# Kernel tuning notes

Measured on AMD Instinct MI355X. Metric: run time of the kernel, lower is better.

Reference implementation:

```python
import jax, jax.numpy as jnp
import numpy as np

B, S, HID = 8, 1024, 1024
NH, HD = 16, 64  # num heads, head dim; NH*HD == HID


def setup_inputs() -> dict:
    key = jax.random.key(0)
    ks = jax.random.split(key, 8)
    sc = 0.02
    return {
        "hidden_states": jax.random.normal(ks[0], (B, S, HID), jnp.float32),
        "attention_mask": jnp.zeros((B, 1, 1, S), jnp.float32),
        "Wq": jax.random.normal(ks[1], (HID, HID), jnp.float32) * sc,
        "bq": jnp.zeros((HID,), jnp.float32),
        "Wk": jax.random.normal(ks[2], (HID, HID), jnp.float32) * sc,
        "bk": jnp.zeros((HID,), jnp.float32),
        "Wv": jax.random.normal(ks[3], (HID, HID), jnp.float32) * sc,
        "bv": jnp.zeros((HID,), jnp.float32),
    }


def reference(hidden_states, attention_mask, Wq, bq, Wk, bk, Wv, bv):
    def split_heads(x):  # [B,S,HID] -> [B,NH,S,HD]
        return x.reshape(B, S, NH, HD).transpose(0, 2, 1, 3)

    q = split_heads(hidden_states @ Wq + bq)
    k = split_heads(hidden_states @ Wk + bk)
    v = split_heads(hidden_states @ Wv + bv)

    # [B,NH,S,S] score matrix, scale, additive mask, softmax
    scores = jnp.einsum("bhqd,bhkd->bhqk", q, k) / jnp.sqrt(jnp.float32(HD))
    scores = scores + attention_mask
    probs = jax.nn.softmax(scores, axis=-1)  # dropout prob = 0.0 -> identity

    ctx = jnp.einsum("bhqk,bhkd->bhqd", probs, v)
    return ctx.transpose(0, 2, 1, 3).reshape(B, S, HID)
```

## Files before the change

### kernel.cpp

```cpp
#include <hip/hip_runtime.h>


typedef __bf16 bf16x8 __attribute__((ext_vector_type(8)));
typedef float f32x16 __attribute__((ext_vector_type(16)));

__device__ __forceinline__ unsigned rne16(float x) {
  unsigned u = __builtin_bit_cast(unsigned, x);
  return (u + 0x7fffu + ((u >> 16) & 1u)) >> 16;
}
__device__ __forceinline__ unsigned packbf(float lo, float hi) {
  return rne16(lo) | (rne16(hi) << 16);
}
__device__ __forceinline__ unsigned packbf_fast(float lo, float hi) {
  unsigned ul = __builtin_bit_cast(unsigned, lo) + 0x8000u;
  unsigned uh = __builtin_bit_cast(unsigned, hi) + 0x8000u;
  return __builtin_amdgcn_perm(uh, ul, 0x07060302u);
}
__device__ __forceinline__ void async16(void* l, const void* g) {
  __builtin_amdgcn_global_load_lds((const __attribute__((address_space(1))) void*)g,
                                   (__attribute__((address_space(3))) void*)l, 16, 0, 0);
}

__global__ __launch_bounds__(256) void k_prep(const float* __restrict__ h,
                                              unsigned short* __restrict__ hbf,
                                              const float* __restrict__ Wq,
                                              const float* __restrict__ Wk,
                                              const float* __restrict__ Wv,
                                              unsigned short* __restrict__ wt) {
  __shared__ float t[32][33];
  int bid = blockIdx.x, tid = threadIdx.x;
  if (bid < 8192) {
    size_t i = (size_t)bid * 256 + tid;
    float4 v = ((const float4*)h)[i];
    uint2 r;
    r.x = packbf(v.x, v.y);
    r.y = packbf(v.z, v.w);
    ((uint2*)hbf)[i] = r;
  } else {
    int id = bid - 8192;
    int which = id >> 10;
    int sub = id & 1023;
    int c0 = (sub & 31) * 32, k0 = (sub >> 5) * 32;
    const float* W = which == 0 ? Wq : (which == 1 ? Wk : Wv);
    int tx = tid & 31, ty = tid >> 5;
#pragma unroll
    for (int i = 0; i < 4; ++i) {
      int r = ty + i * 8;
      t[r][tx] = W[(size_t)(k0 + r) * 1024 + c0 + tx];
    }
    __syncthreads();
#pragma unroll
    for (int i = 0; i < 4; ++i) {
      int r = ty + i * 8;
      wt[((size_t)which * 1024 + c0 + r) * 1024 + k0 + tx] = (unsigned short)rne16(t[tx][r]);
    }
  }
}

__global__ __launch_bounds__(256, 2) void k_gemm(const unsigned short* __restrict__ A,
                                                 const unsigned short* __restrict__ Bm,
                                                 const float* __restrict__ bq,
                                                 const float* __restrict__ bk,
                                                 const float* __restrict__ bv,
                                                 unsigned short* __restrict__ qkv,
                                                 unsigned short* __restrict__ vt) {
  __shared__ __align__(16) char lds[49152];
  int tid = threadIdx.x, w = tid >> 6, lane = tid & 63, l5 = lane & 31, q5 = lane >> 5;
  int wr = w >> 1, wc = w & 1;
  int m0 = blockIdx.x * 256, n0 = blockIdx.y * 128;

  f32x16 acc[4][2];
#pragma unroll
  for (int i = 0; i < 4; ++i)
#pragma unroll
    for (int j = 0; j < 2; ++j)
#pragma unroll
      for (int e = 0; e < 16; ++e) acc[i][j][e] = 0.f;

  auto stage = [&](int kt, char* buf) {
    int k0 = kt * 32;
#pragma unroll
    for (int t = 0; t < 6; ++t) {
      int idx = w * 6 + t;
      if (idx < 16) {
        int mt = idx >> 1, ks = idx & 1;
        async16(buf + idx * 1024,
                A + (size_t)(m0 + mt * 32 + l5) * 1024 + k0 + ks * 16 + q5 * 8);
      } else {
        int i2 = idx - 16, nt = i2 >> 1, ks = i2 & 1;
        async16(buf + 16384 + i2 * 1024,
                Bm + (size_t)(n0 + nt * 32 + l5) * 1024 + k0 + ks * 16 + q5 * 8);
      }
    }
  };

  auto compute = [&](const char* buf) {
#pragma unroll
    for (int ks = 0; ks < 2; ++ks) {
      bf16x8 b0 = *(const bf16x8*)(buf + 16384 + ((wc * 2 + 0) * 2 + ks) * 1024 + lane * 16);
      bf16x8 b1 = *(const bf16x8*)(buf + 16384 + ((wc * 2 + 1) * 2 + ks) * 1024 + lane * 16);
#pragma unroll
      for (int mt = 0; mt < 4; ++mt) {
        bf16x8 a = *(const bf16x8*)(buf + ((wr * 4 + mt) * 2 + ks) * 1024 + lane * 16);
        acc[mt][0] = __builtin_amdgcn_mfma_f32_32x32x16_bf16(a, b0, acc[mt][0], 0, 0, 0);
        acc[mt][1] = __builtin_amdgcn_mfma_f32_32x32x16_bf16(a, b1, acc[mt][1], 0, 0, 0);
      }
    }
  };

  char* buf0 = lds;
  char* buf1 = lds + 24576;
  stage(0, buf0);
#pragma unroll 1
  for (int kt = 0; kt < 32; kt += 2) {
    __syncthreads();
    if (kt + 1 < 32) stage(kt + 1, buf1);
    compute(buf0);
    __syncthreads();
    if (kt + 2 < 32) stage(kt + 2, buf0);
    compute(buf1);
  }

  int which = n0 >> 10;
  if (which != 2) {
    const float* bp = which == 0 ? bq : bk;
    unsigned short* dst = qkv + (size_t)which * 8388608;
#pragma unroll
    for (int nt = 0; nt < 2; ++nt) {
      int n_in = (n0 & 1023) + wc * 64 + nt * 32 + l5;
      float bias = bp[n_in];
      int hh = n_in >> 6, d = n_in & 63;
#pragma unroll
      for (int mt = 0; mt < 4; ++mt) {
#pragma unroll
        for (int e = 0; e < 16; ++e) {
          int m = m0 + wr * 128 + mt * 32 + (e & 3) + 8 * (e >> 2) + 4 * q5;
          int b = m >> 10, s = m & 1023;
          dst[((size_t)(b * 16 + hh) << 16) + (s << 6) + d] =
              (unsigned short)rne16(acc[mt][nt][e] + bias);
        }
      }
    }
  } else {
    int b = m0 >> 10;
    unsigned short* scr = (unsigned short*)(lds) + w * 2176;
#pragma unroll
    for (int mt = 0; mt < 4; ++mt) {
#pragma unroll
      for (int nt = 0; nt < 2; ++nt) {
        int n_in = (n0 & 1023) + wc * 64 + nt * 32 + l5;
        float bias = bv[n_in];
        unsigned short* tile = scr + nt * 1088;
#pragma unroll
        for (int jj = 0; jj < 8; ++jj) {
          int e = 2 * jj;
          int s_loc = (e & 3) + 8 * (e >> 2) + 4 * q5;
          *(unsigned*)(tile + l5 * 34 + s_loc) =
              packbf(acc[mt][nt][e] + bias, acc[mt][nt][e + 1] + bias);
        }
      }
#pragma unroll
      for (int nt = 0; nt < 2; ++nt) {
        const unsigned short* tile = scr + nt * 1088;
        unsigned di[8];
#pragma unroll
        for (int i = 0; i < 8; ++i)
          di[i] = *(const unsigned*)(tile + l5 * 34 + q5 * 16 + i * 2);
        int n_in = (n0 & 1023) + wc * 64 + nt * 32 + l5;
        int hh = n_in >> 6, dd = n_in & 63;
        int s_base = (m0 & 1023) + wr * 128 + mt * 32 + q5 * 16;
        unsigned short* dst = vt + ((size_t)(b * 16 + hh) * 64 + dd) * 1024 + s_base;
        uint4 v0 = {di[0], di[1], di[2], di[3]};
        uint4 v1 = {di[4], di[5], di[6], di[7]};
        *(uint4*)(dst) = v0;
        *(uint4*)(dst + 8) = v1;
      }
    }
  }
}

__global__ __launch_bounds__(256, 4) void k_attn(const unsigned short* __restrict__ qg,
                                                 const unsigned short* __restrict__ kg,
                                                 const unsigned short* __restrict__ vtg,
                                                 const float* __restrict__ maskg,
                                                 float* __restrict__ out) {
  __shared__ __align__(16) char lds[36864];
  char* KF = lds;
  char* VF = lds + 16384;
  float* MK = (float*)(lds + 32768);
  int tid = threadIdx.x, w = tid >> 6, lane = tid & 63, l5 = lane & 31, q5 = lane >> 5;
  int idx = blockIdx.x;
  int bi = idx & 7;
  int j = idx >> 3;
  int h = j >> 3, qc = j & 7;
  int bh = bi * 16 + h, s0 = qc * 128;
  const unsigned short* qb = qg + ((size_t)bh << 16);
  const unsigned short* kb = kg + ((size_t)bh << 16);
  const unsigned short* vb = vtg + ((size_t)bh << 16);
  const float LG = 1.4426950408889634f;
  const float C1 = 0.125f * LG;

  {
    float4 mv = *(const float4*)(maskg + (size_t)bi * 1024 + tid * 4);
    mv.x *= LG; mv.y *= LG; mv.z *= LG; mv.w *= LG;
    *(float4*)(MK + tid * 4) = mv;
  }

  bf16x8 qfr[4];
#pragma unroll
  for (int ds = 0; ds < 4; ++ds)
    qfr[ds] = *(const bf16x8*)(qb + (size_t)(s0 + w * 32 + l5) * 64 + ds * 16 + q5 * 8);

  f32x16 O[2];
#pragma unroll
  for (int i = 0; i < 2; ++i)
#pragma unroll
    for (int e = 0; e < 16; ++e) O[i][e] = 0.f;
  float lsum = 0.f;

#pragma unroll 1
  for (int kt = 0; kt < 8; ++kt) {
    int k0 = kt * 128;
    __syncthreads();
#pragma unroll
    for (int t = 0; t < 4; ++t) {
      int f = w * 4 + t, mt = f >> 2, ds = f & 3;
      async16(KF + f * 1024, kb + (size_t)(k0 + mt * 32 + l5) * 64 + ds * 16 + q5 * 8);
    }
#pragma unroll
    for (int t = 0; t < 4; ++t) {
      int f = w * 4 + t, dt = f >> 3, ks = f & 7;
      async16(VF + f * 1024, vb + (size_t)(dt * 32 + l5) * 1024 + k0 + ks * 16 + q5 * 8);
    }
    __syncthreads();

#pragma unroll
    for (int mt = 0; mt < 4; ++mt) {
      f32x16 S;
#pragma unroll
      for (int e = 0; e < 16; ++e) S[e] = 0.f;
#pragma unroll
      for (int ds = 0; ds < 4; ++ds) {
        bf16x8 a = *(const bf16x8*)(KF + (mt * 4 + ds) * 1024 + lane * 16);
        S = __builtin_amdgcn_mfma_f32_32x32x16_bf16(a, qfr[ds], S, 0, 0, 0);
      }
      float p[16];
#pragma unroll
      for (int g4 = 0; g4 < 4; ++g4) {
        float4 mv = *(const float4*)(MK + k0 + mt * 32 + g4 * 8 + q5 * 4);
        p[g4 * 4 + 0] = __builtin_amdgcn_exp2f(S[g4 * 4 + 0] * C1 + mv.x);
        p[g4 * 4 + 1] = __builtin_amdgcn_exp2f(S[g4 * 4 + 1] * C1 + mv.y);
        p[g4 * 4 + 2] = __builtin_amdgcn_exp2f(S[g4 * 4 + 2] * C1 + mv.z);
        p[g4 * 4 + 3] = __builtin_amdgcn_exp2f(S[g4 * 4 + 3] * C1 + mv.w);
      }
      unsigned p2[8];
#pragma unroll
      for (int e = 0; e < 16; ++e) lsum += p[e];
#pragma unroll
      for (int jj = 0; jj < 8; ++jj) p2[jj] = packbf_fast(p[2 * jj], p[2 * jj + 1]);
#pragma unroll
      for (int kh = 0; kh < 2; ++kh) {
        int ks = mt * 2 + kh, gp = kh * 4;
        bf16x8 av0 = *(const bf16x8*)(VF + (0 * 8 + ks) * 1024 + lane * 16);
        bf16x8 av1 = *(const bf16x8*)(VF + (1 * 8 + ks) * 1024 + lane * 16);
        unsigned o0 = p2[gp + 0], o1 = p2[gp + 1];
        unsigned o2 = p2[gp + 2], o3 = p2[gp + 3];
        unsigned t0 = __shfl_xor((int)o0, 32);
        unsigned t1 = __shfl_xor((int)o1, 32);
        unsigned t2 = __shfl_xor((int)o2, 32);
        unsigned t3 = __shfl_xor((int)o3, 32);
        uint4 fu;
        fu.x = q5 ? t2 : o0;
        fu.y = q5 ? t3 : o1;
        fu.z = q5 ? o2 : t0;
        fu.w = q5 ? o3 : t1;
        bf16x8 bfrag = __builtin_bit_cast(bf16x8, fu);
        O[0] = __builtin_amdgcn_mfma_f32_32x32x16_bf16(av0, bfrag, O[0], 0, 0, 0);
        O[1] = __builtin_amdgcn_mfma_f32_32x32x16_bf16(av1, bfrag, O[1], 0, 0, 0);
      }
    }
  }

  __syncthreads();
  float* Ob = (float*)(lds + w * 8192);
  float lt = lsum + __shfl_xor(lsum, 32);
  float rinv = 1.0f / lt;
#pragma unroll
  for (int dt = 0; dt < 2; ++dt)
#pragma unroll
    for (int g4 = 0; g4 < 4; ++g4) {
      float4 val;
      val.x = O[dt][g4 * 4 + 0] * rinv;
      val.y = O[dt][g4 * 4 + 1] * rinv;
      val.z = O[dt][g4 * 4 + 2] * rinv;
      val.w = O[dt][g4 * 4 + 3] * rinv;
      int c = dt * 8 + g4 * 2 + q5;
      *(float4*)(Ob + l5 * 64 + (c ^ (l5 & 15)) * 4) = val;
    }
#pragma unroll
  for (int t = 0; t < 8; ++t) {
    int qr = t * 4 + (lane >> 4), cr = lane & 15;
    float4 vv = *(const float4*)(Ob + qr * 64 + (cr ^ (qr & 15)) * 4);
    int s = s0 + w * 32 + qr;
    *(float4*)(out + (((size_t)(bi * 1024 + s)) << 10) + (h << 6) + (cr << 2)) = vv;
  }
}

extern "C" void kernel_launch(void* const* d_in, const int* in_sizes, int n_in,
                              void* d_out, int out_size, void* d_ws, size_t ws_size,
                              hipStream_t stream) {
  (void)in_sizes; (void)n_in; (void)out_size; (void)ws_size;
  const float* hidden = (const float*)d_in[0];
  const float* mask = (const float*)d_in[1];
  const float* Wq = (const float*)d_in[2];
  const float* bq = (const float*)d_in[3];
  const float* Wk = (const float*)d_in[4];
  const float* bk = (const float*)d_in[5];
  const float* Wv = (const float*)d_in[6];
  const float* bv = (const float*)d_in[7];
  float* out = (float*)d_out;
  char* ws = (char*)d_ws;
  unsigned short* hbf = (unsigned short*)ws;
  unsigned short* wt  = (unsigned short*)(ws + 16777216);
  unsigned short* qkv = (unsigned short*)(ws + 23068672);
  unsigned short* vt  = (unsigned short*)(ws + 56623104);

  k_prep<<<11264, 256, 0, stream>>>(hidden, hbf, Wq, Wk, Wv, wt);
  k_gemm<<<dim3(32, 24), 256, 0, stream>>>(hbf, wt, bq, bk, bv, qkv, vt);
  k_attn<<<1024, 256, 0, stream>>>(qkv, qkv + 8388608, vt, mask, out);
}
```

Baseline: 254.1 us.

## Rewrite QKV GEMM with 256x256 tiles, 512 threads and swizzled LDS pipelining

The QKV projection GEMM now uses 256x256 output tiles per 512-thread block with 16x16x32 MFMAs. Operands are staged through a 128KB double-buffered, XOR-swizzled LDS layout with interleaved async prefetches, explicit waitcnt/barrier scheduling and setprio around the MFMA bursts. It also remaps block IDs for XCD locality and simplifies the V-transpose epilogue to direct packed stores. This raises data reuse per LDS byte and overlaps loads with compute, at the cost of heavy LDS use that limits occupancy and hand-tuned synchronization that is fragile.

Result: faster. 220.9 us (-13.0%).

```diff
diff --git a/kernel.cpp b/kernel.cpp
--- a/kernel.cpp
+++ b/kernel.cpp
@@ -2,7 +2,9 @@
 
 
 typedef __bf16 bf16x8 __attribute__((ext_vector_type(8)));
+typedef float f32x4 __attribute__((ext_vector_type(4)));
 typedef float f32x16 __attribute__((ext_vector_type(16)));
+typedef int i32x4 __attribute__((ext_vector_type(4)));
 
 __device__ __forceinline__ unsigned rne16(float x) {
   unsigned u = __builtin_bit_cast(unsigned, x);
@@ -19,6 +21,12 @@
 __device__ __forceinline__ void async16(void* l, const void* g) {
   __builtin_amdgcn_global_load_lds((const __attribute__((address_space(1))) void*)g,
                                    (__attribute__((address_space(3))) void*)l, 16, 0, 0);
+}
+__device__ __forceinline__ bf16x8 dsr128(const char* p) {
+  i32x4 r;
+  unsigned a = (unsigned)(size_t)(const __attribute__((address_space(3))) char*)p;
+  asm volatile("ds_read_b128 %0, %1" : "=v"(r) : "v"(a));
+  return __builtin_bit_cast(bf16x8, r);
 }
 
 __global__ __launch_bounds__(256) void k_prep(const float* __restrict__ h,
@@ -57,123 +65,154 @@
   }
 }
 
-__global__ __launch_bounds__(256, 2) void k_gemm(const unsigned short* __restrict__ A,
+__global__ __launch_bounds__(512, 2) void k_gemm(const unsigned short* __restrict__ A,
                                                  const unsigned short* __restrict__ Bm,
                                                  const float* __restrict__ bq,
                                                  const float* __restrict__ bk,
                                                  const float* __restrict__ bv,
                                                  unsigned short* __restrict__ qkv,
                                                  unsigned short* __restrict__ vt) {
-  __shared__ __align__(16) char lds[49152];
-  int tid = threadIdx.x, w = tid >> 6, lane = tid & 63, l5 = lane & 31, q5 = lane >> 5;
-  int wr = w >> 1, wc = w & 1;
-  int m0 = blockIdx.x * 256, n0 = blockIdx.y * 128;
-
-  f32x16 acc[4][2];
-#pragma unroll
-  for (int i = 0; i < 4; ++i)
+  __shared__ __align__(16) char lds[131072];
+  const int tid = threadIdx.x;
+  const int w = tid >> 6, lane = tid & 63;
+  const int wm = w >> 2, wn = w & 3;
+
+  int orig = blockIdx.x;
+  int wgid = (orig & 7) * 48 + (orig >> 3);
+  int tm = wgid / 12, tn = wgid - tm * 12;
+  int m0 = tm * 256, n0 = tn * 256;
+
+  int ro[2], ke[2];
+#pragma unroll
+  for (int j = 0; j < 2; ++j) {
+    int o = j * 8192 + tid * 16;
+    int s = o >> 10, w10 = o & 1023;
+    int lg = w10 ^ (((w10 >> 9) & 1) << 5);
+    ro[j] = ((s >> 1) << 4) + (lg >> 6);
+    ke[j] = ((s & 1) << 5) + ((lg & 63) >> 1);
+  }
+  auto stage_half = [&](int ldsoff, const unsigned short* src, int rb, int k0) {
 #pragma unroll
     for (int j = 0; j < 2; ++j)
-#pragma unroll
-      for (int e = 0; e < 16; ++e) acc[i][j][e] = 0.f;
-
-  auto stage = [&](int kt, char* buf) {
-    int k0 = kt * 32;
-#pragma unroll
-    for (int t = 0; t < 6; ++t) {
-      int idx = w * 6 + t;
-      if (idx < 16) {
-        int mt = idx >> 1, ks = idx & 1;
-        async16(buf + idx * 1024,
-                A + (size_t)(m0 + mt * 32 + l5) * 1024 + k0 + ks * 16 + q5 * 8);
-      } else {
-        int i2 = idx - 16, nt = i2 >> 1, ks = i2 & 1;
-        async16(buf + 16384 + i2 * 1024,
-                Bm + (size_t)(n0 + nt * 32 + l5) * 1024 + k0 + ks * 16 + q5 * 8);
-      }
-    }
+      async16(lds + ldsoff + j * 8192 + w * 1024,
+              src + (size_t)(rb + ro[j]) * 1024 + (k0 + ke[j]));
   };
-
-  auto compute = [&](const char* buf) {
-#pragma unroll
-    for (int ks = 0; ks < 2; ++ks) {
-      bf16x8 b0 = *(const bf16x8*)(buf + 16384 + ((wc * 2 + 0) * 2 + ks) * 1024 + lane * 16);
-      bf16x8 b1 = *(const bf16x8*)(buf + 16384 + ((wc * 2 + 1) * 2 + ks) * 1024 + lane * 16);
-#pragma unroll
-      for (int mt = 0; mt < 4; ++mt) {
-        bf16x8 a = *(const bf16x8*)(buf + ((wr * 4 + mt) * 2 + ks) * 1024 + lane * 16);
-        acc[mt][0] = __builtin_amdgcn_mfma_f32_32x32x16_bf16(a, b0, acc[mt][0], 0, 0, 0);
-        acc[mt][1] = __builtin_amdgcn_mfma_f32_32x32x16_bf16(a, b1, acc[mt][1], 0, 0, 0);
-      }
-    }
+  auto stA = [&](int t) {
+    int d = (t & 1) << 16;
+    stage_half(d, A, m0, t * 64);
+    stage_half(d + 16384, A, m0 + 128, t * 64);
   };
-
-  char* buf0 = lds;
-  char* buf1 = lds + 24576;
-  stage(0, buf0);
+  auto stB0 = [&](int t) { stage_half(((t & 1) << 16) + 32768, Bm, n0, t * 64); };
+  auto stB1 = [&](int t) { stage_half(((t & 1) << 16) + 49152, Bm, n0 + 128, t * 64); };
+
+  const int lswz = (((lane & 15) << 6) | ((lane >> 4) << 4)) ^ ((lane & 8) << 2);
+
+  f32x4 acc[8][4];
+#pragma unroll
+  for (int i = 0; i < 8; ++i)
+#pragma unroll
+    for (int j = 0; j < 4; ++j)
+#pragma unroll
+      for (int e = 0; e < 4; ++e) acc[i][j][e] = 0.f;
+
+  stA(0); stB0(0); stB1(0); stB0(1); stB1(1);
+  asm volatile("s_waitcnt vmcnt(4)");
+  __builtin_amdgcn_s_barrier();
+  __builtin_amdgcn_sched_barrier(0);
+
 #pragma unroll 1
-  for (int kt = 0; kt < 32; kt += 2) {
-    __syncthreads();
-    if (kt + 1 < 32) stage(kt + 1, buf1);
-    compute(buf0);
-    __syncthreads();
-    if (kt + 2 < 32) stage(kt + 2, buf0);
-    compute(buf1);
-  }
-
-  int which = n0 >> 10;
+  for (int it = 0; it < 8; ++it) {
+    const int u = it * 2;
+    const bool pf = it < 7;
+#pragma unroll
+    for (int G = 0; G < 2; ++G) {
+      const char* abase = lds + (G << 16) + wm * 16384 + lswz;
+      const char* bbase = lds + (G << 16) + 32768 + (wn >> 1) * 16384 + ((wn & 1) << 13) + lswz;
+      bf16x8 bF[4][2];
+#pragma unroll
+      for (int ph = 0; ph < 4; ++ph) {
+        if (ph == 0) {
+#pragma unroll
+          for (int n = 0; n < 4; ++n)
+#pragma unroll
+            for (int ks = 0; ks < 2; ++ks)
+              bF[n][ks] = dsr128(bbase + (n * 2 + ks) * 1024);
+        }
+        bf16x8 aF[2][2];
+#pragma unroll
+        for (int mm = 0; mm < 2; ++mm)
+#pragma unroll
+          for (int ks = 0; ks < 2; ++ks)
+            aF[mm][ks] = dsr128(abase + ((ph * 2 + mm) * 2 + ks) * 1024);
+        if (G == 0) {
+          if (ph == 0) stA(u + 1);
+          else if (ph == 1) { if (pf) stB0(u + 2); }
+          else if (ph == 2) { if (pf) stB1(u + 2); }
+        } else {
+          if (ph == 0) { if (pf) stA(u + 2); }
+          else if (ph == 1) { if (pf) stB0(u + 3); }
+          else if (ph == 2) { if (pf) stB1(u + 3); }
+        }
+        __builtin_amdgcn_s_barrier();
+        asm volatile("s_waitcnt lgkmcnt(0)");
+        __builtin_amdgcn_sched_barrier(0);
+        __builtin_amdgcn_s_setprio(1);
+#pragma unroll
+        for (int ks = 0; ks < 2; ++ks)
+#pragma unroll
+          for (int mm = 0; mm < 2; ++mm)
+#pragma unroll
+            for (int n = 0; n < 4; ++n)
+              acc[ph * 2 + mm][n] = __builtin_amdgcn_mfma_f32_16x16x32_bf16(
+                  aF[mm][ks], bF[n][ks], acc[ph * 2 + mm][n], 0, 0, 0);
+        __builtin_amdgcn_s_setprio(0);
+        if (ph == 3) {
+          if (G == 0) {
+            if (pf) asm volatile("s_waitcnt vmcnt(4)");
+            else    asm volatile("s_waitcnt vmcnt(0)");
+          } else {
+            if (pf) asm volatile("s_waitcnt vmcnt(4)");
+          }
+        }
+        __builtin_amdgcn_s_barrier();
+        __builtin_amdgcn_sched_barrier(0);
+      }
+    }
+  }
+
+  const int which = tn >> 2;
+  const int ng = n0 & 1023;
+  const int b = m0 >> 10;
+  const int r = lane & 15, qq = lane >> 4;
+  const int sb = (m0 & 1023) + wm * 128 + qq * 4;
+
   if (which != 2) {
     const float* bp = which == 0 ? bq : bk;
-    unsigned short* dst = qkv + (size_t)which * 8388608;
-#pragma unroll
-    for (int nt = 0; nt < 2; ++nt) {
-      int n_in = (n0 & 1023) + wc * 64 + nt * 32 + l5;
+    unsigned short* base = qkv + ((size_t)which << 23) + ((size_t)b << 20);
+#pragma unroll
+    for (int n = 0; n < 4; ++n) {
+      int n_in = ng + wn * 64 + n * 16 + r;
       float bias = bp[n_in];
-      int hh = n_in >> 6, d = n_in & 63;
-#pragma unroll
-      for (int mt = 0; mt < 4; ++mt) {
-#pragma unroll
-        for (int e = 0; e < 16; ++e) {
-          int m = m0 + wr * 128 + mt * 32 + (e & 3) + 8 * (e >> 2) + 4 * q5;
-          int b = m >> 10, s = m & 1023;
-          dst[((size_t)(b * 16 + hh) << 16) + (s << 6) + d] =
-              (unsigned short)rne16(acc[mt][nt][e] + bias);
-        }
-      }
+      unsigned short* dp = base + ((size_t)(n_in >> 6) << 16) + (n_in & 63);
+#pragma unroll
+      for (int m = 0; m < 8; ++m)
+#pragma unroll
+        for (int e = 0; e < 4; ++e)
+          dp[(size_t)(sb + m * 16 + e) << 6] = (unsigned short)rne16(acc[m][n][e] + bias);
     }
   } else {
-    int b = m0 >> 10;
-    unsigned short* scr = (unsigned short*)(lds) + w * 2176;
-#pragma unroll
-    for (int mt = 0; mt < 4; ++mt) {
-#pragma unroll
-      for (int nt = 0; nt < 2; ++nt) {
-        int n_in = (n0 & 1023) + wc * 64 + nt * 32 + l5;
-        float bias = bv[n_in];
-        unsigned short* tile = scr + nt * 1088;
-#pragma unroll
-        for (int jj = 0; jj < 8; ++jj) {
-          int e = 2 * jj;
-          int s_loc = (e & 3) + 8 * (e >> 2) + 4 * q5;
-          *(unsigned*)(tile + l5 * 34 + s_loc) =
-              packbf(acc[mt][nt][e] + bias, acc[mt][nt][e + 1] + bias);
-        }
-      }
-#pragma unroll
-      for (int nt = 0; nt < 2; ++nt) {
-        const unsigned short* tile = scr + nt * 1088;
-        unsigned di[8];
-#pragma unroll
-        for (int i = 0; i < 8; ++i)
-          di[i] = *(const unsigned*)(tile + l5 * 34 + q5 * 16 + i * 2);
-        int n_in = (n0 & 1023) + wc * 64 + nt * 32 + l5;
-        int hh = n_in >> 6, dd = n_in & 63;
-        int s_base = (m0 & 1023) + wr * 128 + mt * 32 + q5 * 16;
-        unsigned short* dst = vt + ((size_t)(b * 16 + hh) * 64 + dd) * 1024 + s_base;
-        uint4 v0 = {di[0], di[1], di[2], di[3]};
-        uint4 v1 = {di[4], di[5], di[6], di[7]};
-        *(uint4*)(dst) = v0;
-        *(uint4*)(dst + 8) = v1;
+    unsigned short* vbase = vt + ((size_t)b << 20);
+#pragma unroll
+    for (int n = 0; n < 4; ++n) {
+      int n_in = ng + wn * 64 + n * 16 + r;
+      float bias = bv[n_in];
+      unsigned short* dp = vbase + ((size_t)n_in << 10) + sb;
+#pragma unroll
+      for (int m = 0; m < 8; ++m) {
+        uint2 pk;
+        pk.x = packbf(acc[m][n][0] + bias, acc[m][n][1] + bias);
+        pk.y = packbf(acc[m][n][2] + bias, acc[m][n][3] + bias);
+        *(uint2*)(dp + m * 16) = pk;
       }
     }
   }
@@ -326,6 +365,6 @@
   unsigned short* vt  = (unsigned short*)(ws + 56623104);
 
   k_prep<<<11264, 256, 0, stream>>>(hidden, hbf, Wq, Wk, Wv, wt);
-  k_gemm<<<dim3(32, 24), 256, 0, stream>>>(hbf, wt, bq, bk, bv, qkv, vt);
+  k_gemm<<<384, 512, 0, stream>>>(hbf, wt, bq, bk, bv, qkv, vt);
   k_attn<<<1024, 256, 0, stream>>>(qkv, qkv + 8388608, vt, mask, out);
 }
```
